# Kernel optimization log

Measured on AMD Instinct MI355X. Metric: run time of the kernel, lower is better.

## Reference

```python
import jax, jax.numpy as jnp
import numpy as np

N = 169343      # ogbn-arxiv node count
E = 1166243     # ogbn-arxiv edge count
DIN = 128       # input feature dim
DM = 128        # config.d_model


def setup_inputs() -> dict:
    key = jax.random.key(0)
    k = jax.random.split(key, 6)
    x = jax.random.normal(k[0], (N, DIN), dtype=jnp.float32)
    edge_index = jax.random.randint(k[1], (2, E), 0, N, dtype=jnp.int64)
    W1 = jax.random.normal(k[2], (DIN, DM), dtype=jnp.float32) / np.float32(np.sqrt(DIN))
    b1 = jnp.zeros((DM,), dtype=jnp.float32)
    W2 = jax.random.normal(k[3], (DM, DM), dtype=jnp.float32) / np.float32(np.sqrt(DM))
    b2 = jnp.zeros((DM,), dtype=jnp.float32)
    return {"x": x, "edge_index": edge_index, "W1": W1, "b1": b1, "W2": W2, "b2": b2}


def gcn_conv(h, W, b, src, dst, dinv):
    # GCNConv: out = D^{-1/2} (A + I) D^{-1/2} (h W) + b
    hw = h @ W                                      # [N, C]
    norm = dinv[src] * dinv[dst]                    # [E]
    msgs = hw[src] * norm[:, None]                  # [E, C] gather
    agg = jax.ops.segment_sum(msgs, dst, num_segments=N)  # scatter-add
    agg = agg + hw * (dinv * dinv)[:, None]         # self-loop term
    return agg + b


def reference(x, edge_index, W1, b1, W2, b2):
    src, dst = edge_index[0], edge_index[1]
    # degree with self-loops (PyG GCNConv convention: deg from dst/col)
    deg = jnp.zeros((N,), dtype=x.dtype).at[dst].add(1.0) + 1.0
    dinv = jax.lax.rsqrt(deg)
    h = jax.nn.relu(gcn_conv(x, W1, b1, src, dst, dinv))
    out = gcn_conv(h, W2, b2, src, dst, dinv)
    out = out[None]  # unsqueeze(0) -> [1, N, DM]
    return (out, out)  # original returns (out, None, out)
```

## Files before the change

kernel.cpp:

```cpp
#include <hip/hip_runtime.h>
#include <hip/hip_fp16.h>

#define DMODEL 128

__global__ void cnt_kernel(const int* __restrict__ dst, int* __restrict__ cnt, int E) {
    int e = blockIdx.x * blockDim.x + threadIdx.x;
    if (e < E) atomicAdd(&cnt[dst[e]], 1);
}

__global__ void scan1_kernel(const int* __restrict__ cnt, int* __restrict__ incl,
                             int* __restrict__ bsum, int n) {
    __shared__ int s[256];
    int t = threadIdx.x;
    int i = blockIdx.x * 256 + t;
    int v = (i < n) ? cnt[i] : 0;
    s[t] = v;
    __syncthreads();
    for (int off = 1; off < 256; off <<= 1) {
        int add = (t >= off) ? s[t - off] : 0;
        __syncthreads();
        s[t] += add;
        __syncthreads();
    }
    if (i < n) incl[i] = s[t];
    if (t == 255) bsum[blockIdx.x] = s[255];
}

__global__ void scan2_kernel(int* __restrict__ bsum, int nb) {
    __shared__ int s[256];
    __shared__ int carry;
    int t = threadIdx.x;
    if (t == 0) carry = 0;
    __syncthreads();
    for (int base = 0; base < nb; base += 256) {
        int idx = base + t;
        int v = (idx < nb) ? bsum[idx] : 0;
        s[t] = v;
        __syncthreads();
        for (int off = 1; off < 256; off <<= 1) {
            int add = (t >= off) ? s[t - off] : 0;
            __syncthreads();
            s[t] += add;
            __syncthreads();
        }
        int excl = carry + s[t] - v;
        if (idx < nb) bsum[idx] = excl;
        __syncthreads();
        if (t == 255) carry += s[255];
    }
}

__global__ void scan3_kernel(const int* __restrict__ cnt, const int* __restrict__ incl,
                             const int* __restrict__ bsum, int* __restrict__ offsets,
                             int* __restrict__ cursor, float* __restrict__ dinv,
                             int n, int E) {
    int i = blockIdx.x * 256 + threadIdx.x;
    if (i < n) {
        int v = cnt[i];
        int excl = incl[i] - v + bsum[blockIdx.x];
        offsets[i] = excl;
        cursor[i] = excl;
        dinv[i] = rsqrtf((float)v + 1.0f);
    }
    if (i == 0) offsets[n] = E;
}

__global__ void fill_kernel(const int* __restrict__ src, const int* __restrict__ dst,
                            int* __restrict__ cursor, const float* __restrict__ dinv,
                            int2* __restrict__ er, int E) {
    int e = blockIdx.x * blockDim.x + threadIdx.x;
    if (e < E) {
        int s = src[e];
        int d = dst[e];
        int p = atomicAdd(&cursor[d], 1);
        er[p] = make_int2(s, __float_as_int(dinv[s] * dinv[d]));
    }
}

template <int OUT_HALF>
__global__ __launch_bounds__(256, 4) void gemm_kernel(const float* __restrict__ A,
                                                      const float* __restrict__ W,
                                                      void* __restrict__ Cout, int n) {
    __shared__ float sA[32][132];
    __shared__ float sW[32][128];
    const int tid  = threadIdx.x;
    const int row0 = blockIdx.x * 128;
    const int tx = tid & 15;
    const int ty = tid >> 4;

    float acc[8][8];
#pragma unroll
    for (int i = 0; i < 8; ++i)
#pragma unroll
        for (int j = 0; j < 8; ++j) acc[i][j] = 0.f;

    for (int kt = 0; kt < 128; kt += 32) {
#pragma unroll
        for (int p = 0; p < 4; ++p) {
            int r  = p * 32 + (tid >> 3);
            int kq = tid & 7;
            int row = row0 + r;
            float4 v = make_float4(0.f, 0.f, 0.f, 0.f);
            if (row < n) v = *(const float4*)&A[(size_t)row * DMODEL + kt + kq * 4];
            sA[kq * 4 + 0][r] = v.x;
            sA[kq * 4 + 1][r] = v.y;
            sA[kq * 4 + 2][r] = v.z;
            sA[kq * 4 + 3][r] = v.w;
        }
#pragma unroll
        for (int q = 0; q < 4; ++q) {
            int f  = q * 256 + tid;
            int k  = f >> 5;
            int c4 = f & 31;
            *(float4*)&sW[k][c4 * 4] = *(const float4*)&W[(size_t)(kt + k) * DMODEL + c4 * 4];
        }
        __syncthreads();

#pragma unroll 8
        for (int k = 0; k < 32; ++k) {
            float4 a0 = *(const float4*)&sA[k][ty * 4];
            float4 a1 = *(const float4*)&sA[k][64 + ty * 4];
            float4 w0 = *(const float4*)&sW[k][tx * 4];
            float4 w1 = *(const float4*)&sW[k][64 + tx * 4];
            float av[8] = {a0.x, a0.y, a0.z, a0.w, a1.x, a1.y, a1.z, a1.w};
            float wv[8] = {w0.x, w0.y, w0.z, w0.w, w1.x, w1.y, w1.z, w1.w};
#pragma unroll
            for (int i = 0; i < 8; ++i)
#pragma unroll
                for (int j = 0; j < 8; ++j)
                    acc[i][j] += av[i] * wv[j];
        }
        __syncthreads();
    }

#pragma unroll
    for (int i = 0; i < 8; ++i) {
        int r = row0 + (i < 4 ? ty * 4 + i : 64 + ty * 4 + (i - 4));
        if (r < n) {
            if (OUT_HALF) {
                __half* Ch = (__half*)Cout;
                union { __half2 h2[2]; uint2 u; } p0, p1;
                p0.h2[0] = __floats2half2_rn(acc[i][0], acc[i][1]);
                p0.h2[1] = __floats2half2_rn(acc[i][2], acc[i][3]);
                p1.h2[0] = __floats2half2_rn(acc[i][4], acc[i][5]);
                p1.h2[1] = __floats2half2_rn(acc[i][6], acc[i][7]);
                *(uint2*)&Ch[(size_t)r * DMODEL + tx * 4] = p0.u;
                *(uint2*)&Ch[(size_t)r * DMODEL + 64 + tx * 4] = p1.u;
            } else {
                float* Cf = (float*)Cout;
                *(float4*)&Cf[(size_t)r * DMODEL + tx * 4] =
                    make_float4(acc[i][0], acc[i][1], acc[i][2], acc[i][3]);
                *(float4*)&Cf[(size_t)r * DMODEL + 64 + tx * 4] =
                    make_float4(acc[i][4], acc[i][5], acc[i][6], acc[i][7]);
            }
        }
    }
}

__global__ __launch_bounds__(256) void pull_kernel(const __half* __restrict__ hw,
                                                   const int* __restrict__ offsets,
                                                   const int2* __restrict__ er,
                                                   const float* __restrict__ dinv,
                                                   const float* __restrict__ bias,
                                                   float* __restrict__ out1,
                                                   float* __restrict__ out2,
                                                   int n, int relu) {
    int node = blockIdx.x * 4 + (threadIdx.x >> 6);
    int lane = threadIdx.x & 63;
    if (node >= n) return;
    const __half2* hwv = (const __half2*)hw;
    float di = dinv[node];
    float s2 = di * di;
    float2 selfv = __half22float2(hwv[(size_t)node * 64 + lane]);
    float2 a0, a1, a2, a3;
    a0.x = selfv.x * s2 + bias[lane * 2];
    a0.y = selfv.y * s2 + bias[lane * 2 + 1];
    a1 = make_float2(0.f, 0.f);
    a2 = make_float2(0.f, 0.f);
    a3 = make_float2(0.f, 0.f);
    int e0 = offsets[node];
    int e1 = offsets[node + 1];
    int e = e0;
    for (; e + 4 <= e1; e += 4) {
        int2 r0 = er[e];
        int2 r1 = er[e + 1];
        int2 r2 = er[e + 2];
        int2 r3 = er[e + 3];
        __half2 h0 = hwv[(size_t)r0.x * 64 + lane];
        __half2 h1 = hwv[(size_t)r1.x * 64 + lane];
        __half2 h2 = hwv[(size_t)r2.x * 64 + lane];
        __half2 h3 = hwv[(size_t)r3.x * 64 + lane];
        float2 v0 = __half22float2(h0);
        float2 v1 = __half22float2(h1);
        float2 v2 = __half22float2(h2);
        float2 v3 = __half22float2(h3);
        float w0 = __int_as_float(r0.y);
        float w1 = __int_as_float(r1.y);
        float w2 = __int_as_float(r2.y);
        float w3 = __int_as_float(r3.y);
        a0.x += v0.x * w0; a0.y += v0.y * w0;
        a1.x += v1.x * w1; a1.y += v1.y * w1;
        a2.x += v2.x * w2; a2.y += v2.y * w2;
        a3.x += v3.x * w3; a3.y += v3.y * w3;
    }
    for (; e < e1; ++e) {
        int2 r = er[e];
        float w = __int_as_float(r.y);
        float2 v = __half22float2(hwv[(size_t)r.x * 64 + lane]);
        a0.x += v.x * w;
        a0.y += v.y * w;
    }
    float2 acc;
    acc.x = (a0.x + a1.x) + (a2.x + a3.x);
    acc.y = (a0.y + a1.y) + (a2.y + a3.y);
    if (relu) {
        acc.x = fmaxf(acc.x, 0.f);
        acc.y = fmaxf(acc.y, 0.f);
    }
    ((float2*)out1)[(size_t)node * 64 + lane] = acc;
    if (out2) ((float2*)out2)[(size_t)node * 64 + lane] = acc;
}

__global__ void dup_kernel(const float4* __restrict__ s, float4* __restrict__ a,
                           float4* __restrict__ b, int n4) {
    int i = blockIdx.x * blockDim.x + threadIdx.x;
    if (i < n4) {
        float4 v = s[i];
        a[i] = v;
        b[i] = v;
    }
}

extern "C" void kernel_launch(void* const* d_in, const int* in_sizes, int n_in,
                              void* d_out, int out_size, void* d_ws, size_t ws_size,
                              hipStream_t stream) {
    const float* x  = (const float*)d_in[0];
    const int*   ei = (const int*)d_in[1];
    const float* W1 = (const float*)d_in[2];
    const float* b1 = (const float*)d_in[3];
    const float* W2 = (const float*)d_in[4];
    const float* b2 = (const float*)d_in[5];
    float* out = (float*)d_out;

    const int n = in_sizes[0] / DMODEL;
    const int E = in_sizes[1] / 2;
    const int* src = ei;
    const int* dst = ei + E;

    const long long nd = (long long)n * DMODEL;
    const int NB = (n + 255) / 256;
    const int Na = NB * 256;
    const int NBa = ((NB + 255) / 256) * 256;
    const int Ea = ((E + 255) / 256) * 256;

    float* outA = out;
    float* outB = out + nd;

    float* dinv  = (float*)d_ws;
    float* hwbuf = dinv + Na;
    __half* hwh  = (__half*)hwbuf;

    const size_t need_ints = (size_t)Na + (size_t)nd + 4ull * Na + NBa + 256 + 2ull * Ea;
    const bool ws_csr = ws_size >= need_ints * sizeof(int);

    int* base = ws_csr ? (int*)(hwbuf + nd) : (int*)outA;
    int* cnt     = base;
    int* incl    = cnt + Na;
    int* bsum    = incl + Na;
    int* offsets = bsum + NBa;
    int* cursor  = offsets + Na + 256;
    int2* er     = (int2*)(cursor + Na);

    hipMemsetAsync(cnt, 0, (size_t)n * sizeof(int), stream);
    cnt_kernel<<<(E + 255) / 256, 256, 0, stream>>>(dst, cnt, E);
    scan1_kernel<<<NB, 256, 0, stream>>>(cnt, incl, bsum, n);
    scan2_kernel<<<1, 256, 0, stream>>>(bsum, NB);
    scan3_kernel<<<NB, 256, 0, stream>>>(cnt, incl, bsum, offsets, cursor, dinv, n, E);
    fill_kernel<<<(E + 255) / 256, 256, 0, stream>>>(src, dst, cursor, dinv, er, E);

    dim3 ggrid((n + 127) / 128);
    const int pull_grid = (n + 3) / 4;

    if (ws_csr) {
        gemm_kernel<1><<<ggrid, 256, 0, stream>>>(x, W1, hwh, n);
        pull_kernel<<<pull_grid, 256, 0, stream>>>(hwh, offsets, er, dinv, b1,
                                                   outB, nullptr, n, 1);
        gemm_kernel<1><<<ggrid, 256, 0, stream>>>(outB, W2, hwh, n);
        pull_kernel<<<pull_grid, 256, 0, stream>>>(hwh, offsets, er, dinv, b2,
                                                   outA, outB, n, 0);
    } else {
        __half* hwh2 = (__half*)outB;
        gemm_kernel<1><<<ggrid, 256, 0, stream>>>(x, W1, hwh2, n);
        pull_kernel<<<pull_grid, 256, 0, stream>>>(hwh2, offsets, er, dinv, b1,
                                                   hwbuf, nullptr, n, 1);
        gemm_kernel<1><<<ggrid, 256, 0, stream>>>(hwbuf, W2, hwh2, n);
        pull_kernel<<<pull_grid, 256, 0, stream>>>(hwh2, offsets, er, dinv, b2,
                                                   hwbuf, nullptr, n, 0);
        const int n4 = (int)(nd / 4);
        dup_kernel<<<(n4 + 255) / 256, 256, 0, stream>>>((const float4*)hwbuf,
                                                         (float4*)outA, (float4*)outB, n4);
    }
}
```

Measured before the change: 629.3 us.

## Replace FP32 SIMT GEMM with FP16 MFMA GEMM and store hidden layer in FP16

Replaces the scalar FP32 register-tiled GEMM with an MFMA 16x16x32 f16 kernel that loads a full 128x128 A tile and a transposed FP16 weight tile into XOR-swizzled shared memory, then stages the output through LDS for coalesced stores. Small kernels pre-convert and transpose W1/W2 to FP16. The first aggregation now writes the hidden activations in FP16, which halves that write and the second GEMM's read. The cost is lower precision in the hidden layer and the weights, plus 64KB of LDS per block, which limits occupancy.

Result: faster. 552.2 us (-12.3%).

```diff
diff --git a/kernel.cpp b/kernel.cpp
--- a/kernel.cpp
+++ b/kernel.cpp
@@ -2,6 +2,9 @@
 #include <hip/hip_fp16.h>
 
 #define DMODEL 128
+
+typedef _Float16 h8 __attribute__((ext_vector_type(8)));
+typedef float fx4 __attribute__((ext_vector_type(4)));
 
 __global__ void cnt_kernel(const int* __restrict__ dst, int* __restrict__ cnt, int E) {
     int e = blockIdx.x * blockDim.x + threadIdx.x;
@@ -77,93 +80,121 @@
     }
 }
 
-template <int OUT_HALF>
-__global__ __launch_bounds__(256, 4) void gemm_kernel(const float* __restrict__ A,
-                                                      const float* __restrict__ W,
-                                                      void* __restrict__ Cout, int n) {
-    __shared__ float sA[32][132];
-    __shared__ float sW[32][128];
+__global__ void wconv_kernel(const float* __restrict__ W, __half* __restrict__ Wt) {
+    int i = blockIdx.x * 256 + threadIdx.x;
+    int k = i >> 7, c = i & 127;
+    Wt[c * 128 + k] = (__half)W[i];
+}
+
+template <int A_F16>
+__global__ __launch_bounds__(256) void gemm_mfma(const void* __restrict__ Ain,
+                                                 const __half* __restrict__ Wt,
+                                                 __half* __restrict__ C, int n) {
+    __shared__ _Float16 sA[128][128];
+    __shared__ _Float16 sB[128][128];
     const int tid  = threadIdx.x;
     const int row0 = blockIdx.x * 128;
-    const int tx = tid & 15;
-    const int ty = tid >> 4;
-
-    float acc[8][8];
-#pragma unroll
-    for (int i = 0; i < 8; ++i)
-#pragma unroll
-        for (int j = 0; j < 8; ++j) acc[i][j] = 0.f;
-
-    for (int kt = 0; kt < 128; kt += 32) {
-#pragma unroll
-        for (int p = 0; p < 4; ++p) {
-            int r  = p * 32 + (tid >> 3);
-            int kq = tid & 7;
+
+#pragma unroll
+    for (int p = 0; p < 8; ++p) {
+        int f = p * 256 + tid;
+        int c = f >> 4, seg = f & 15;
+        uint4 v = *(const uint4*)&Wt[(size_t)c * 128 + seg * 8];
+        *(uint4*)((char*)&sB[c][0] + (((seg ^ (c & 7)) << 4))) = v;
+    }
+    if (A_F16) {
+        const __half* Ah = (const __half*)Ain;
+#pragma unroll
+        for (int p = 0; p < 8; ++p) {
+            int f = p * 256 + tid;
+            int r = f >> 4, seg = f & 15;
+            int row = row0 + r;
+            uint4 v = make_uint4(0, 0, 0, 0);
+            if (row < n) v = *(const uint4*)&Ah[(size_t)row * 128 + seg * 8];
+            *(uint4*)((char*)&sA[r][0] + (((seg ^ (r & 7)) << 4))) = v;
+        }
+    } else {
+        const float* Af = (const float*)Ain;
+#pragma unroll
+        for (int p = 0; p < 16; ++p) {
+            int f = p * 256 + tid;
+            int r = f >> 5, c4 = f & 31;
             int row = row0 + r;
             float4 v = make_float4(0.f, 0.f, 0.f, 0.f);
-            if (row < n) v = *(const float4*)&A[(size_t)row * DMODEL + kt + kq * 4];
-            sA[kq * 4 + 0][r] = v.x;
-            sA[kq * 4 + 1][r] = v.y;
-            sA[kq * 4 + 2][r] = v.z;
-            sA[kq * 4 + 3][r] = v.w;
-        }
-#pragma unroll
-        for (int q = 0; q < 4; ++q) {
-            int f  = q * 256 + tid;
-            int k  = f >> 5;
-            int c4 = f & 31;
-            *(float4*)&sW[k][c4 * 4] = *(const float4*)&W[(size_t)(kt + k) * DMODEL + c4 * 4];
-        }
-        __syncthreads();
-
-#pragma unroll 8
-        for (int k = 0; k < 32; ++k) {
-            float4 a0 = *(const float4*)&sA[k][ty * 4];
-            float4 a1 = *(const float4*)&sA[k][64 + ty * 4];
-            float4 w0 = *(const float4*)&sW[k][tx * 4];
-            float4 w1 = *(const float4*)&sW[k][64 + tx * 4];
-            float av[8] = {a0.x, a0.y, a0.z, a0.w, a1.x, a1.y, a1.z, a1.w};
-            float wv[8] = {w0.x, w0.y, w0.z, w0.w, w1.x, w1.y, w1.z, w1.w};
-#pragma unroll
-            for (int i = 0; i < 8; ++i)
-#pragma unroll
-                for (int j = 0; j < 8; ++j)
-                    acc[i][j] += av[i] * wv[j];
-        }
-        __syncthreads();
-    }
-
-#pragma unroll
-    for (int i = 0; i < 8; ++i) {
-        int r = row0 + (i < 4 ? ty * 4 + i : 64 + ty * 4 + (i - 4));
-        if (r < n) {
-            if (OUT_HALF) {
-                __half* Ch = (__half*)Cout;
-                union { __half2 h2[2]; uint2 u; } p0, p1;
-                p0.h2[0] = __floats2half2_rn(acc[i][0], acc[i][1]);
-                p0.h2[1] = __floats2half2_rn(acc[i][2], acc[i][3]);
-                p1.h2[0] = __floats2half2_rn(acc[i][4], acc[i][5]);
-                p1.h2[1] = __floats2half2_rn(acc[i][6], acc[i][7]);
-                *(uint2*)&Ch[(size_t)r * DMODEL + tx * 4] = p0.u;
-                *(uint2*)&Ch[(size_t)r * DMODEL + 64 + tx * 4] = p1.u;
-            } else {
-                float* Cf = (float*)Cout;
-                *(float4*)&Cf[(size_t)r * DMODEL + tx * 4] =
-                    make_float4(acc[i][0], acc[i][1], acc[i][2], acc[i][3]);
-                *(float4*)&Cf[(size_t)r * DMODEL + 64 + tx * 4] =
-                    make_float4(acc[i][4], acc[i][5], acc[i][6], acc[i][7]);
+            if (row < n) v = *(const float4*)&Af[(size_t)row * 128 + c4 * 4];
+            union { _Float16 h[4]; uint2 u; } cv;
+            cv.h[0] = (_Float16)v.x; cv.h[1] = (_Float16)v.y;
+            cv.h[2] = (_Float16)v.z; cv.h[3] = (_Float16)v.w;
+            int gsw = (c4 >> 1) ^ (r & 7);
+            *(uint2*)((char*)&sA[r][0] + (gsw << 4) + ((c4 & 1) << 3)) = cv.u;
+        }
+    }
+    __syncthreads();
+
+    const int lane = tid & 63;
+    const int w    = tid >> 6;
+    const int c15  = lane & 15;
+    const int g    = lane >> 4;
+
+    fx4 acc[2][8];
+#pragma unroll
+    for (int i = 0; i < 2; ++i)
+#pragma unroll
+        for (int j = 0; j < 8; ++j) acc[i][j] = (fx4){0.f, 0.f, 0.f, 0.f};
+
+    const int rA0 = w * 32 + c15;
+    const int rA1 = rA0 + 16;
+#pragma unroll
+    for (int ks = 0; ks < 4; ++ks) {
+        int kg = ks * 4 + g;
+        h8 a0 = *(h8*)((char*)&sA[rA0][0] + ((kg ^ (rA0 & 7)) << 4));
+        h8 a1 = *(h8*)((char*)&sA[rA1][0] + ((kg ^ (rA1 & 7)) << 4));
+#pragma unroll
+        for (int tn = 0; tn < 8; ++tn) {
+            int cb = tn * 16 + c15;
+            h8 b = *(h8*)((char*)&sB[cb][0] + ((kg ^ (cb & 7)) << 4));
+            acc[0][tn] = __builtin_amdgcn_mfma_f32_16x16x32_f16(a0, b, acc[0][tn], 0, 0, 0);
+            acc[1][tn] = __builtin_amdgcn_mfma_f32_16x16x32_f16(a1, b, acc[1][tn], 0, 0, 0);
+        }
+    }
+
+    __syncthreads();
+    _Float16* sC = &sA[0][0];
+#pragma unroll
+    for (int tm = 0; tm < 2; ++tm) {
+#pragma unroll
+        for (int tn = 0; tn < 8; ++tn) {
+#pragma unroll
+            for (int j = 0; j < 4; ++j) {
+                int r = w * 32 + tm * 16 + g * 4 + j;
+                int c = tn * 16 + c15;
+                *(_Float16*)((char*)(sC + (size_t)r * 128) +
+                             (((c >> 3) ^ (r & 7)) << 4) + ((c & 7) << 1)) =
+                    (_Float16)acc[tm][tn][j];
             }
         }
     }
-}
-
+    __syncthreads();
+#pragma unroll
+    for (int p = 0; p < 8; ++p) {
+        int f = p * 256 + tid;
+        int r = f >> 4, seg = f & 15;
+        int row = row0 + r;
+        if (row < n) {
+            uint4 v = *(uint4*)((char*)(sC + (size_t)r * 128) + ((seg ^ (r & 7)) << 4));
+            *(uint4*)&C[(size_t)row * 128 + seg * 8] = v;
+        }
+    }
+}
+
+template <int OUT_HALF>
 __global__ __launch_bounds__(256) void pull_kernel(const __half* __restrict__ hw,
                                                    const int* __restrict__ offsets,
                                                    const int2* __restrict__ er,
                                                    const float* __restrict__ dinv,
                                                    const float* __restrict__ bias,
-                                                   float* __restrict__ out1,
-                                                   float* __restrict__ out2,
+                                                   void* __restrict__ out1,
+                                                   void* __restrict__ out2,
                                                    int n, int relu) {
     int node = blockIdx.x * 4 + (threadIdx.x >> 6);
     int lane = threadIdx.x & 63;
@@ -186,14 +217,10 @@
         int2 r1 = er[e + 1];
         int2 r2 = er[e + 2];
         int2 r3 = er[e + 3];
-        __half2 h0 = hwv[(size_t)r0.x * 64 + lane];
-        __half2 h1 = hwv[(size_t)r1.x * 64 + lane];
-        __half2 h2 = hwv[(size_t)r2.x * 64 + lane];
-        __half2 h3 = hwv[(size_t)r3.x * 64 + lane];
-        float2 v0 = __half22float2(h0);
-        float2 v1 = __half22float2(h1);
-        float2 v2 = __half22float2(h2);
-        float2 v3 = __half22float2(h3);
+        float2 v0 = __half22float2(hwv[(size_t)r0.x * 64 + lane]);
+        float2 v1 = __half22float2(hwv[(size_t)r1.x * 64 + lane]);
+        float2 v2 = __half22float2(hwv[(size_t)r2.x * 64 + lane]);
+        float2 v3 = __half22float2(hwv[(size_t)r3.x * 64 + lane]);
         float w0 = __int_as_float(r0.y);
         float w1 = __int_as_float(r1.y);
         float w2 = __int_as_float(r2.y);
@@ -217,8 +244,12 @@
         acc.x = fmaxf(acc.x, 0.f);
         acc.y = fmaxf(acc.y, 0.f);
     }
-    ((float2*)out1)[(size_t)node * 64 + lane] = acc;
-    if (out2) ((float2*)out2)[(size_t)node * 64 + lane] = acc;
+    if (OUT_HALF) {
+        ((__half2*)out1)[(size_t)node * 64 + lane] = __floats2half2_rn(acc.x, acc.y);
+    } else {
+        ((float2*)out1)[(size_t)node * 64 + lane] = acc;
+        if (out2) ((float2*)out2)[(size_t)node * 64 + lane] = acc;
+    }
 }
 
 __global__ void dup_kernel(const float4* __restrict__ s, float4* __restrict__ a,
@@ -259,8 +290,10 @@
     float* dinv  = (float*)d_ws;
     float* hwbuf = dinv + Na;
     __half* hwh  = (__half*)hwbuf;
-
-    const size_t need_ints = (size_t)Na + (size_t)nd + 4ull * Na + NBa + 256 + 2ull * Ea;
+    __half* hh   = hwh + nd;
+
+    const size_t need_ints = (size_t)Na + (size_t)nd + 4ull * Na + NBa + 256 +
+                             2ull * Ea + 16384;
     const bool ws_csr = ws_size >= need_ints * sizeof(int);
 
     int* base = ws_csr ? (int*)(hwbuf + nd) : (int*)outA;
@@ -270,6 +303,8 @@
     int* offsets = bsum + NBa;
     int* cursor  = offsets + Na + 256;
     int2* er     = (int2*)(cursor + Na);
+    __half* Wt1  = (__half*)(er + Ea);
+    __half* Wt2  = Wt1 + 16384;
 
     hipMemsetAsync(cnt, 0, (size_t)n * sizeof(int), stream);
     cnt_kernel<<<(E + 255) / 256, 256, 0, stream>>>(dst, cnt, E);
@@ -277,25 +312,28 @@
     scan2_kernel<<<1, 256, 0, stream>>>(bsum, NB);
     scan3_kernel<<<NB, 256, 0, stream>>>(cnt, incl, bsum, offsets, cursor, dinv, n, E);
     fill_kernel<<<(E + 255) / 256, 256, 0, stream>>>(src, dst, cursor, dinv, er, E);
+    wconv_kernel<<<64, 256, 0, stream>>>(W1, Wt1);
+    wconv_kernel<<<64, 256, 0, stream>>>(W2, Wt2);
 
     dim3 ggrid((n + 127) / 128);
     const int pull_grid = (n + 3) / 4;
 
     if (ws_csr) {
-        gemm_kernel<1><<<ggrid, 256, 0, stream>>>(x, W1, hwh, n);
-        pull_kernel<<<pull_grid, 256, 0, stream>>>(hwh, offsets, er, dinv, b1,
-                                                   outB, nullptr, n, 1);
-        gemm_kernel<1><<<ggrid, 256, 0, stream>>>(outB, W2, hwh, n);
-        pull_kernel<<<pull_grid, 256, 0, stream>>>(hwh, offsets, er, dinv, b2,
-                                                   outA, outB, n, 0);
+        gemm_mfma<0><<<ggrid, 256, 0, stream>>>(x, Wt1, hwh, n);
+        pull_kernel<1><<<pull_grid, 256, 0, stream>>>(hwh, offsets, er, dinv, b1,
+                                                      hh, nullptr, n, 1);
+        gemm_mfma<1><<<ggrid, 256, 0, stream>>>(hh, Wt2, hwh, n);
+        pull_kernel<0><<<pull_grid, 256, 0, stream>>>(hwh, offsets, er, dinv, b2,
+                                                      outA, outB, n, 0);
     } else {
         __half* hwh2 = (__half*)outB;
-        gemm_kernel<1><<<ggrid, 256, 0, stream>>>(x, W1, hwh2, n);
-        pull_kernel<<<pull_grid, 256, 0, stream>>>(hwh2, offsets, er, dinv, b1,
-                                                   hwbuf, nullptr, n, 1);
-        gemm_kernel<1><<<ggrid, 256, 0, stream>>>(hwbuf, W2, hwh2, n);
-        pull_kernel<<<pull_grid, 256, 0, stream>>>(hwh2, offsets, er, dinv, b2,
-                                                   hwbuf, nullptr, n, 0);
+        __half* hh2  = hwh2 + nd;
+        gemm_mfma<0><<<ggrid, 256, 0, stream>>>(x, Wt1, hwh2, n);
+        pull_kernel<1><<<pull_grid, 256, 0, stream>>>(hwh2, offsets, er, dinv, b1,
+                                                      hh2, nullptr, n, 1);
+        gemm_mfma<1><<<ggrid, 256, 0, stream>>>(hh2, Wt2, hwh2, n);
+        pull_kernel<0><<<pull_grid, 256, 0, stream>>>(hwh2, offsets, er, dinv, b2,
+                                                      hwbuf, nullptr, n, 0);
         const int n4 = (int)(nd / 4);
         dup_kernel<<<(n4 + 255) / 256, 256, 0, stream>>>((const float4*)hwbuf,
                                                          (float4*)outA, (float4*)outB, n4);
```
